# Performance work log

Measured on AMD Instinct MI355X. Metric: run time of the kernel, lower is better.

## Reference

```python
import jax, jax.numpy as jnp
import numpy as np

B, N, R, CIN = 2, 2048, 128, 256
RADIUS, NSAMPLE, OUT = 0.3, 16, 5
EPS = 1e-5


def setup_inputs():
    key = jax.random.key(0)
    ks = jax.random.split(key, 8)
    points_xyz = jax.random.uniform(ks[0], (B, N, 3)) * 2.0          # scene ~2m cube
    features = jax.random.normal(ks[1], (B, CIN, N))
    ctr = jax.random.uniform(ks[2], (B, R, 3)) * 2.0
    size = jax.random.uniform(ks[3], (B, R, 3)) * 0.6 + 0.3          # positive box sizes
    ang = jax.random.uniform(ks[4], (B, R, 1)) * np.pi
    rois = jnp.concatenate([ctr, size, ang], axis=-1)                # [B,R,7]
    s = 0.02
    W_mlp = jax.random.normal(ks[5], (256, CIN + 3)) * s
    g_mlp = jnp.ones((256,)); bt_mlp = jnp.zeros((256,))
    W1 = jax.random.normal(ks[6], (128, 256)) * s; b1 = jnp.zeros((128,))
    g1 = jnp.ones((128,)); bt1 = jnp.zeros((128,))
    W2 = jax.random.normal(ks[7], (128, 128)) * s; b2 = jnp.zeros((128,))
    g2 = jnp.ones((128,)); bt2 = jnp.zeros((128,))
    return dict(points_xyz=points_xyz, features=features, rois=rois,
                W_mlp=W_mlp, g_mlp=g_mlp, bt_mlp=bt_mlp,
                W1=W1, b1=b1, g1=g1, bt1=bt1,
                W2=W2, b2=b2, g2=g2, bt2=bt2)


def _bn(x, g, b, axes, shape):
    # training-mode BatchNorm (batch statistics), matching torch .train() forward
    m = jnp.mean(x, axes, keepdims=True)
    v = jnp.var(x, axes, keepdims=True)
    return (x - m) * jax.lax.rsqrt(v + EPS) * g.reshape(shape) + b.reshape(shape)


def _forward(points_xyz, features, rois, W_mlp, g_mlp, bt_mlp,
             W1, b1, g1, bt1, W2, b2, g2, bt2):
    # ---- QueryAndGroup: ball query (min_radius=0) + gather + center + normalize_xyz ----
    diff = points_xyz[:, :, None, :] - points_xyz[:, None, :, :]     # [B,Nq,Np,3]
    d2 = jnp.sum(diff * diff, -1)
    mask = d2 < RADIUS * RADIUS
    cand = jnp.where(mask, jnp.arange(N, dtype=jnp.int32)[None, None, :], N)
    idx = jnp.sort(cand, axis=-1)[..., :NSAMPLE]                     # first NSAMPLE in-ball, ascending point index
    idx = jnp.where(idx < N, idx, idx[..., :1])                      # pad with first valid (self always in-ball)
    gx = jax.vmap(lambda p, i: p[i])(points_xyz, idx)                # [B,N,S,3]
    gx = (gx - points_xyz[:, :, None, :]) / RADIUS                   # centered + normalized
    gf = jax.vmap(lambda f, i: f[i])(jnp.swapaxes(features, 1, 2), idx)  # [B,N,S,C]
    nf = jnp.transpose(jnp.concatenate([gx, gf], -1), (0, 3, 1, 2))  # [B,3+C,N,S] (use_xyz=True)
    # ---- mlp: Conv2d 1x1 (bias='auto' with BN -> no bias) + BN2d + ReLU ----
    h = jnp.einsum('oc,bcns->bons', W_mlp, nf)
    h = jax.nn.relu(_bn(h, g_mlp, bt_mlp, (0, 2, 3), (1, -1, 1, 1)))
    feats = jnp.max(h, -1)                                           # max_pool2d over samples -> [B,256,N]
    h = jnp.einsum('oc,bcn->bon', W1, feats) + b1[None, :, None]
    h = jax.nn.relu(_bn(h, g1, bt1, (0, 2), (1, -1, 1)))
    h = jnp.einsum('oc,bcn->bon', W2, h) + b2[None, :, None]
    feats = jax.nn.relu(_bn(h, g2, bt2, (0, 2), (1, -1, 1)))         # [B,128,N]
    # ---- RoIPool3d: roi-aware voxel max pool (out_size=5, mode='max') ----
    C = feats.shape[1]
    ctr, size, ry = rois[..., :3], rois[..., 3:6], rois[..., 6]
    rel = points_xyz[:, None, :, :] - ctr[:, :, None, :]             # [B,R,N,3]
    c = jnp.cos(ry)[:, :, None]; s = jnp.sin(ry)[:, :, None]
    lx = rel[..., 0] * c + rel[..., 1] * s                           # rotate by -ry into roi frame
    ly = -rel[..., 0] * s + rel[..., 1] * c
    local = jnp.stack([lx, ly, rel[..., 2]], -1)                     # [B,R,N,3]
    half = size[:, :, None, :] * 0.5
    inside = jnp.all(jnp.abs(local) < half, -1)                      # [B,R,N]
    v = jnp.clip(jnp.floor((local + half) / (2.0 * half) * OUT), 0, OUT - 1).astype(jnp.int32)
    vox = (v[..., 0] * OUT + v[..., 1]) * OUT + v[..., 2]
    base = jnp.arange(B * R, dtype=jnp.int32).reshape(B, R, 1) * (OUT ** 3)
    seg = jnp.where(inside, base + vox, B * R * OUT ** 3).reshape(-1)  # dummy segment for outside pts
    data = jnp.broadcast_to(jnp.swapaxes(feats, 1, 2)[:, None], (B, R, N, C)).reshape(-1, C)
    pooled = jax.ops.segment_max(data, seg, num_segments=B * R * OUT ** 3 + 1)[:-1]
    pooled = jnp.where(jnp.isneginf(pooled), 0.0, pooled)            # empty voxels -> 0
    roi_feats = pooled.reshape(B, R, OUT, OUT, OUT, C)
    return feats, roi_feats


def reference(points_xyz, features, rois, W_mlp, g_mlp, bt_mlp,
              W1, b1, g1, bt1, W2, b2, g2, bt2):
    return _forward(points_xyz, features, rois, W_mlp, g_mlp, bt_mlp,
                    W1, b1, g1, bt1, W2, b2, g2, bt2)
```

## Files before the change

kernel.cpp:

```cpp
#include <hip/hip_runtime.h>
#include <hip/hip_bf16.h>

typedef __hip_bfloat16 bf16;
typedef unsigned short u16;

#define NB   2
#define NPT  2048
#define NROI 128
#define CINF 256
#define NS   16
#define KDIM 259
#define KP2  288
#define C1   256
#define C2   128
#define NVOX 125
#define EPSF 1e-5f

typedef __bf16 bf16x8 __attribute__((ext_vector_type(8)));
typedef float  f32x4  __attribute__((ext_vector_type(4)));

__device__ __forceinline__ float ldin(const void* p, size_t i, int f32flag) {
    if (f32flag) return ((const float*)p)[i];
    unsigned short u = ((const unsigned short*)p)[i];
    return __uint_as_float(((unsigned)u) << 16);
}

__device__ __forceinline__ unsigned short f2bf(float x) {
    unsigned u = __float_as_uint(x);
    u += 0x7FFFu + ((u >> 16) & 1u);
    return (unsigned short)(u >> 16);
}

__device__ __forceinline__ int detect_flag(const void* __restrict__ Wm) {
    const uint4* p = (const uint4*)Wm;
    int bad = 0;
    #pragma unroll
    for (int i = 0; i < 8; i++) {
        uint4 v = p[i];
        unsigned w[4] = {v.x, v.y, v.z, v.w};
        #pragma unroll
        for (int j = 0; j < 4; j++) {
            if (!(fabsf(__uint_as_float(w[j] << 16)) <= 1e4f)) bad = 1;
            if (!(fabsf(__uint_as_float(w[j] & 0xFFFF0000u)) <= 1e4f)) bad = 1;
        }
    }
    return bad;
}


__global__ __launch_bounds__(256) void k_setup(
    const void* __restrict__ pts, const void* __restrict__ feat, const void* __restrict__ rois,
    const void* __restrict__ Wm, const void* __restrict__ gm, const void* __restrict__ btm,
    const void* __restrict__ W1, const void* __restrict__ b1, const void* __restrict__ g1,
    const void* __restrict__ bt1, const void* __restrict__ W2, const void* __restrict__ b2,
    const void* __restrict__ g2, const void* __restrict__ bt2,
    float* __restrict__ ptsf, float* __restrict__ roisf, float* __restrict__ params,
    u16* __restrict__ wbf, u16* __restrict__ w1bf, u16* __restrict__ w2bf,
    float* __restrict__ stats, u16* __restrict__ ftbf,
    float* __restrict__ psx, float* __restrict__ psy, float* __restrict__ psz) {
    int f = detect_flag(Wm);
    int bx = blockIdx.x;
    int tid = threadIdx.x;
    if (bx < 1024) {
        __shared__ float tile[32][33];
        int b = bx >> 9;
        int r = bx & 511;
        int n0 = (r & 63) * 32, c0 = (r >> 6) * 32;
        int tx = tid & 31, ty = tid >> 5;
        #pragma unroll
        for (int d = 0; d < 4; d++) {
            int c = c0 + ty + d * 8;
            tile[ty + d * 8][tx] = ldin(feat, ((size_t)(b * CINF + c)) * NPT + n0 + tx, f);
        }
        __syncthreads();
        #pragma unroll
        for (int d = 0; d < 4; d++) {
            int n = n0 + ty + d * 8;
            ftbf[((size_t)(b * NPT + n)) * CINF + c0 + tx] = f2bf(tile[tx][ty + d * 8]);
        }
    } else if (bx < 1312) {
        int e = (bx - 1024) * 256 + tid;
        int o = e / KP2, k = e % KP2;
        float v = 0.f;
        if (k < 256)      v = ldin(Wm, (size_t)o * KDIM + 3 + k, f);
        else if (k < 259) v = ldin(Wm, (size_t)o * KDIM + (k - 256), f);
        wbf[e] = f2bf(v);
    } else if (bx < 1440) {
        int e = (bx - 1312) * 256 + tid;
        w1bf[e] = f2bf(ldin(W1, e, f));
    } else if (bx < 1504) {
        int e = (bx - 1440) * 256 + tid;
        w2bf[e] = f2bf(ldin(W2, e, f));
    } else if (bx < 1552) {
        int e = (bx - 1504) * 256 + tid;
        if (e < NB * NPT * 3) ptsf[e] = ldin(pts, e, f);
    } else if (bx < 1559) {
        int e = (bx - 1552) * 256 + tid;
        if (e < NB * NROI * 7) roisf[e] = ldin(rois, e, f);
    } else if (bx < 1567) {
        int t = bx - 1559;
        const void* src; int off, n;
        switch (t) {
            case 0: src = gm;  off = 0;     n = 256; break;
            case 1: src = btm; off = 256;   n = 256; break;
            case 2: src = b1;  off = 33280; n = 128; break;
            case 3: src = g1;  off = 33408; n = 128; break;
            case 4: src = bt1; off = 33536; n = 128; break;
            case 5: src = b2;  off = 50048; n = 128; break;
            case 6: src = g2;  off = 50176; n = 128; break;
            default: src = bt2; off = 50304; n = 128; break;
        }
        if (tid < n) params[off + tid] = ldin(src, tid, f);
    } else if (bx < 1570) {
        int e = (bx - 1567) * 256 + tid;
        if (e < 768) {
            int d = e >> 8, o = e & 255;
            params[25088 + e] = ldin(Wm, (size_t)o * KDIM + d, f);
        }
    } else if (bx < 1586) {
        int e = (bx - 1570) * 256 + tid;
        if (e < NB * NPT) {
            psx[e] = ptsf ? ldin(pts, e * 3 + 0, f) : 0.f;
            psy[e] = ldin(pts, e * 3 + 1, f);
            psz[e] = ldin(pts, e * 3 + 2, f);
        }
    } else {
        int e = (bx - 1586) * 256 + tid;
        if (e < 1024) stats[e] = 0.f;
    }
}

__global__ __launch_bounds__(256) void k_qd(const float* __restrict__ psx, const float* __restrict__ psy,
                                            const float* __restrict__ psz, int* __restrict__ idxb,
                                            const u16* __restrict__ ftbf, const u16* __restrict__ wbf,
                                            float* __restrict__ Hf) {
    int bx = blockIdx.x;
    if (bx < 1024) {
        #pragma clang fp contract(off)
        int wid = threadIdx.x >> 6, lane = threadIdx.x & 63;
        int q = bx * 4 + wid;
        int b = q >> 11;
        int base = b * NPT;
        float qx = psx[q], qy = psy[q], qz = psz[q];
        const float R2 = (float)(0.3 * 0.3);
        size_t ob = (size_t)q * NS;
        int cnt = 0, j0 = -1;
        unsigned long long below = (lane == 63) ? ~0ull >> 1 : ((1ull << (lane + 1)) - 1) >> 1;
        for (int c0 = 0; c0 < NPT; c0 += 64) {
            int j = c0 + lane;
            float dx = qx - psx[base + j];
            float dy = qy - psy[base + j];
            float dz = qz - psz[base + j];
            float d2 = dx * dx + dy * dy + dz * dz;
            bool hit = d2 < R2;
            unsigned long long m = __ballot(hit);
            if (m) {
                if (j0 < 0) j0 = c0 + __builtin_ctzll(m);
                int pos = cnt + __popcll(m & below);
                if (hit && pos < NS) idxb[ob + pos] = j;
                cnt += __popcll(m);
            }
            if (cnt >= NS) break;
        }
        if (lane >= cnt && lane < NS) idxb[ob + lane] = j0;
    } else {
        int bx2 = bx - 1024;
        int w = threadIdx.x >> 6, lane = threadIdx.x & 63;
        int lg = lane >> 4, lr = lane & 15;
        int rbase = (bx2 & 255) * 16;
        int c0 = (bx2 >> 8) * 128 + w * 32;

        size_t aoff  = (size_t)(rbase + lr) * CINF + lg * 8;
        size_t boff0 = (size_t)(c0 + lr) * KP2 + lg * 8;
        size_t boff1 = (size_t)(c0 + 16 + lr) * KP2 + lg * 8;

        f32x4 acc0 = (f32x4){0.f, 0.f, 0.f, 0.f};
        f32x4 acc1 = (f32x4){0.f, 0.f, 0.f, 0.f};
        #pragma unroll
        for (int k0 = 0; k0 < 256; k0 += 32) {
            bf16x8 af = __builtin_bit_cast(bf16x8, *(const uint4*)(ftbf + aoff + k0));
            bf16x8 b0 = __builtin_bit_cast(bf16x8, *(const uint4*)(wbf + boff0 + k0));
            bf16x8 b1 = __builtin_bit_cast(bf16x8, *(const uint4*)(wbf + boff1 + k0));
            acc0 = __builtin_amdgcn_mfma_f32_16x16x32_bf16(af, b0, acc0, 0, 0, 0);
            acc1 = __builtin_amdgcn_mfma_f32_16x16x32_bf16(af, b1, acc1, 0, 0, 0);
        }
        #pragma unroll
        for (int r = 0; r < 4; r++) {
            int row = rbase + lg * 4 + r;
            Hf[(size_t)row * C1 + c0 + lr] = acc0[r];
            Hf[(size_t)row * C1 + c0 + 16 + lr] = acc1[r];
        }
    }
}

#define GPTS 8
__global__ __launch_bounds__(256) void k_gather(const float* __restrict__ Hf, const int* __restrict__ idxb,
                                                const float* __restrict__ ptsf, const float* __restrict__ wxyz,
                                                float* __restrict__ Hmax, float* __restrict__ Hmin,
                                                float* __restrict__ stats) {
    __shared__ int   lj[NS];
    __shared__ float lgx[NS], lgy[NS], lgz[NS];
    int o = threadIdx.x;
    float wx = wxyz[o], wy = wxyz[256 + o], wz = wxyz[512 + o];
    float ssum = 0.f, ssq = 0.f;
    for (int p = 0; p < GPTS; p++) {
        int pt = blockIdx.x * GPTS + p;
        int b = pt >> 11;
        int base = b * NPT;
        if (o < NS) {
            int j = idxb[(size_t)pt * NS + o];
            lj[o] = j;
            size_t jb = ((size_t)(base + j)) * 3;
            size_t cb = (size_t)pt * 3;
            lgx[o] = (ptsf[jb]     - ptsf[cb])     / 0.3f;
            lgy[o] = (ptsf[jb + 1] - ptsf[cb + 1]) / 0.3f;
            lgz[o] = (ptsf[jb + 2] - ptsf[cb + 2]) / 0.3f;
        }
        __syncthreads();
        float mx = -3.4e38f, mn = 3.4e38f;
        #pragma unroll
        for (int s = 0; s < NS; s++) {
            float v = Hf[(size_t)(base + lj[s]) * C1 + o] + wx * lgx[s] + wy * lgy[s] + wz * lgz[s];
            mx = fmaxf(mx, v); mn = fminf(mn, v);
            ssum += v; ssq += v * v;
        }
        Hmax[(size_t)pt * C1 + o] = mx;
        Hmin[(size_t)pt * C1 + o] = mn;
        __syncthreads();
    }
    atomicAdd(&stats[o], ssum);
    atomicAdd(&stats[256 + o], ssq);
}

__global__ __launch_bounds__(256) void k_lin1f(const float* __restrict__ Hmax, const float* __restrict__ Hmin,
                                               const float* __restrict__ stats, const float* __restrict__ g,
                                               const float* __restrict__ bt, const u16* __restrict__ Wb,
                                               const float* __restrict__ bias, float* __restrict__ out,
                                               float* __restrict__ sum, float* __restrict__ sumsq) {
    __shared__ __align__(16) u16 xa[16][264];
    int tid = threadIdx.x;
    int rbase = blockIdx.x * 16;
    {
        int c = tid;
        const float inv = 1.f / 65536.f;
        float m = stats[c] * inv;
        float var = fmaxf(stats[256 + c] * inv - m * m, 0.f);
        float a = g[c] / sqrtf(var + EPSF);
        float d = bt[c] - m * a;
        #pragma unroll
        for (int r = 0; r < 16; r++) {
            size_t e = (size_t)(rbase + r) * C1 + c;
            float h = (a > 0.f) ? Hmax[e] : Hmin[e];
            xa[r][c] = f2bf(fmaxf(a * h + d, 0.f));
        }
    }
    __syncthreads();
    int w = tid >> 6, lane = tid & 63;
    int lg = lane >> 4, lr = lane & 15;
    int c0 = w * 32;
    size_t boff0 = (size_t)(c0 + lr) * 256 + lg * 8;
    size_t boff1 = (size_t)(c0 + 16 + lr) * 256 + lg * 8;

    f32x4 acc0 = (f32x4){0.f, 0.f, 0.f, 0.f};
    f32x4 acc1 = (f32x4){0.f, 0.f, 0.f, 0.f};
    #pragma unroll
    for (int k0 = 0; k0 < 256; k0 += 32) {
        bf16x8 af = __builtin_bit_cast(bf16x8, *(const uint4*)&xa[lr][k0 + lg * 8]);
        bf16x8 b0 = __builtin_bit_cast(bf16x8, *(const uint4*)(Wb + boff0 + k0));
        bf16x8 b1 = __builtin_bit_cast(bf16x8, *(const uint4*)(Wb + boff1 + k0));
        acc0 = __builtin_amdgcn_mfma_f32_16x16x32_bf16(af, b0, acc0, 0, 0, 0);
        acc1 = __builtin_amdgcn_mfma_f32_16x16x32_bf16(af, b1, acc1, 0, 0, 0);
    }
    #pragma unroll
    for (int ct = 0; ct < 2; ct++) {
        f32x4 a = ct ? acc1 : acc0;
        int col = c0 + ct * 16 + lr;
        float bi = bias[col];
        float s = 0.f, q = 0.f;
        #pragma unroll
        for (int r = 0; r < 4; r++) {
            float h = a[r] + bi;
            out[(size_t)(rbase + lg * 4 + r) * C2 + col] = h;
            s += h; q += h * h;
        }
        s += __shfl_xor(s, 16); s += __shfl_xor(s, 32);
        q += __shfl_xor(q, 16); q += __shfl_xor(q, 32);
        if (lane < 16) {
            atomicAdd(&sum[col], s);
            atomicAdd(&sumsq[col], q);
        }
    }
}

__global__ __launch_bounds__(256) void k_lin2f(const float* __restrict__ h1, const float* __restrict__ stats1,
                                               const float* __restrict__ g, const float* __restrict__ bt,
                                               const u16* __restrict__ Wb, const float* __restrict__ bias,
                                               float* __restrict__ out, float* __restrict__ sum,
                                               float* __restrict__ sumsq) {
    __shared__ __align__(16) u16 xa[16][136];
    int tid = threadIdx.x;
    int rbase = blockIdx.x * 16;
    {
        int c = tid & 127, half = tid >> 7;
        const float inv = 1.f / 4096.f;
        float m = stats1[c] * inv;
        float var = fmaxf(stats1[128 + c] * inv - m * m, 0.f);
        float a = g[c] / sqrtf(var + EPSF);
        float d = bt[c] - m * a;
        #pragma unroll
        for (int rr = 0; rr < 8; rr++) {
            int r = half * 8 + rr;
            float h = h1[(size_t)(rbase + r) * C2 + c];
            xa[r][c] = f2bf(fmaxf(a * h + d, 0.f));
        }
    }
    __syncthreads();
    int w = tid >> 6, lane = tid & 63;
    int lg = lane >> 4, lr = lane & 15;
    int c0 = w * 32;
    size_t boff0 = (size_t)(c0 + lr) * 128 + lg * 8;
    size_t boff1 = (size_t)(c0 + 16 + lr) * 128 + lg * 8;

    f32x4 acc0 = (f32x4){0.f, 0.f, 0.f, 0.f};
    f32x4 acc1 = (f32x4){0.f, 0.f, 0.f, 0.f};
    #pragma unroll
    for (int k0 = 0; k0 < 128; k0 += 32) {
        bf16x8 af = __builtin_bit_cast(bf16x8, *(const uint4*)&xa[lr][k0 + lg * 8]);
        bf16x8 b0 = __builtin_bit_cast(bf16x8, *(const uint4*)(Wb + boff0 + k0));
        bf16x8 b1 = __builtin_bit_cast(bf16x8, *(const uint4*)(Wb + boff1 + k0));
        acc0 = __builtin_amdgcn_mfma_f32_16x16x32_bf16(af, b0, acc0, 0, 0, 0);
        acc1 = __builtin_amdgcn_mfma_f32_16x16x32_bf16(af, b1, acc1, 0, 0, 0);
    }
    #pragma unroll
    for (int ct = 0; ct < 2; ct++) {
        f32x4 a = ct ? acc1 : acc0;
        int col = c0 + ct * 16 + lr;
        float bi = bias[col];
        float s = 0.f, q = 0.f;
        #pragma unroll
        for (int r = 0; r < 4; r++) {
            float h = a[r] + bi;
            out[(size_t)(rbase + lg * 4 + r) * C2 + col] = h;
            s += h; q += h * h;
        }
        s += __shfl_xor(s, 16); s += __shfl_xor(s, 32);
        q += __shfl_xor(q, 16); q += __shfl_xor(q, 32);
        if (lane < 16) {
            atomicAdd(&sum[col], s);
            atomicAdd(&sumsq[col], q);
        }
    }
}

__global__ void k_final(const float* __restrict__ h2, const float* __restrict__ sum,
                        const float* __restrict__ sumsq, const float* __restrict__ g,
                        const float* __restrict__ bt, float* __restrict__ fp,
                        void* __restrict__ out0, const void* __restrict__ Wm) {
    int e = blockIdx.x * 256 + threadIdx.x;
    if (e >= NB * NPT * C2) return;
    int f = detect_flag(Wm);
    int o = e & (C2 - 1);
    int bn = e >> 7;
    int b = bn >> 11, n = bn & (NPT - 1);
    const float inv = 1.f / 4096.f;
    float m = sum[o] * inv;
    float var = fmaxf(sumsq[o] * inv - m * m, 0.f);
    float a = g[o] / sqrtf(var + EPSF);
    float d = bt[o] - m * a;
    float v = fmaxf(a * h2[e] + d, 0.f);
    fp[e] = v;
    size_t oi = ((size_t)(b * C2 + o)) * NPT + n;
    if (f) ((float*)out0)[oi] = v;
    else   ((unsigned short*)out0)[oi] = f2bf(v);
}

__global__ __launch_bounds__(512) void k_pool2(const float* __restrict__ ptsf, const float* __restrict__ roisf,
                                               const float* __restrict__ fp, void* __restrict__ d_out,
                                               const void* __restrict__ Wm, int* __restrict__ glist) {
    #pragma clang fp contract(off)
    __shared__ int pooled[NVOX * C2];
    __shared__ int cnt;
    __shared__ float rp[8];
    int f = detect_flag(Wm);
    int bid = blockIdx.x;
    int b = bid >> 7;
    int tid = threadIdx.x;
    for (int k = tid; k < NVOX * C2; k += 512) pooled[k] = 0;
    if (tid == 0) {
        cnt = 0;
        size_t rb = ((size_t)bid) * 7;
        rp[0] = roisf[rb];     rp[1] = roisf[rb + 1]; rp[2] = roisf[rb + 2];
        rp[3] = roisf[rb + 3] * 0.5f;
        rp[4] = roisf[rb + 4] * 0.5f;
        rp[5] = roisf[rb + 5] * 0.5f;
        float ry = roisf[rb + 6];
        rp[6] = (float)cos((double)ry);
        rp[7] = (float)sin((double)ry);
    }
    __syncthreads();
    float cx = rp[0], cy = rp[1], cz = rp[2];
    float hx = rp[3], hy = rp[4], hz = rp[5];
    float cf = rp[6], sf = rp[7];
    int* mylist = glist + bid * NPT;
    for (int n = tid; n < NPT; n += 512) {
        size_t pb = ((size_t)(b * NPT + n)) * 3;
        float rx  = ptsf[pb]     - cx;
        float ryy = ptsf[pb + 1] - cy;
        float rz  = ptsf[pb + 2] - cz;
        float lx = rx * cf + ryy * sf;
        float ly = -rx * sf + ryy * cf;
        if (fabsf(lx) < hx && fabsf(ly) < hy && fabsf(rz) < hz) {
            int vx = (int)fminf(fmaxf(floorf((lx + hx) / (2.f * hx) * 5.f), 0.f), 4.f);
            int vy = (int)fminf(fmaxf(floorf((ly + hy) / (2.f * hy) * 5.f), 0.f), 4.f);
            int vz = (int)fminf(fmaxf(floorf((rz + hz) / (2.f * hz) * 5.f), 0.f), 4.f);
            int vox = (vx * 5 + vy) * 5 + vz;
            int pos = atomicAdd(&cnt, 1);
            mylist[pos] = (vox << 16) | n;
        }
    }
    __syncthreads();
    int m = cnt;
    int c = tid & 127, slot = tid >> 7;
    for (int e = slot; e < m; e += 4) {
        int u = mylist[e];
        int n = u & 0xFFFF, vox = u >> 16;
        float v = fp[((size_t)(b * NPT + n)) * C2 + c];
        atomicMax(&pooled[vox * C2 + c], __float_as_int(v));
    }
    __syncthreads();
    size_t ob = (size_t)524288 + (size_t)bid * (NVOX * C2);
    for (int k = tid; k < NVOX * C2; k += 512) {
        float v = __int_as_float(pooled[k]);
        if (f) ((float*)d_out)[ob + k] = v;
        else   ((unsigned short*)d_out)[ob + k] = f2bf(v);
    }
}

extern "C" void kernel_launch(void* const* d_in, const int* in_sizes, int n_in,
                              void* d_out, int out_size, void* d_ws, size_t ws_size,
                              hipStream_t stream) {
    const void* pts  = d_in[0];
    const void* feat = d_in[1];
    const void* rois = d_in[2];
    const void* Wm   = d_in[3];
    const void* gm   = d_in[4];
    const void* btm  = d_in[5];
    const void* W1   = d_in[6];
    const void* b1   = d_in[7];
    const void* g1   = d_in[8];
    const void* bt1  = d_in[9];
    const void* W2   = d_in[10];
    const void* b2   = d_in[11];
    const void* g2   = d_in[12];
    const void* bt2  = d_in[13];

    float* ws     = (float*)d_ws;
    float* ptsf   = ws + 16;
    float* roisf  = ws + 12304;
    float* params = ws + 14096;
    u16*   w1bf   = (u16*)(params + 512);
    u16*   w2bf   = (u16*)(params + 512 + 16384);
    float* wxyz   = params + 25088;
    u16*   wbf    = (u16*)(ws + 64528);
    float* stats  = ws + 101392;
    int*   idxb   = (int*)(ws + 102416);
    u16*   ftbf   = (u16*)(ws + 167952);
    float* Hmax   = ws + 1216528;
    float* Hmin   = ws + 2265104;
    float* h1     = ws + 1216528;
    float* h2     = ws + 2265104;
    float* fp     = ws + 2789392;
    float* psx    = ws + 3313680;
    float* psy    = ws + 3317776;
    float* psz    = ws + 3321872;
    float* Hf     = ws + 3325968;
    int*   glist  = (int*)(ws + 3325968);

    k_setup<<<1590, 256, 0, stream>>>(pts, feat, rois, Wm, gm, btm, W1, b1, g1, bt1,
                                      W2, b2, g2, bt2, ptsf, roisf, params,
                                      wbf, w1bf, w2bf, stats, ftbf, psx, psy, psz);
    k_qd<<<1536, 256, 0, stream>>>(psx, psy, psz, idxb, ftbf, wbf, Hf);
    k_gather<<<(NB * NPT) / GPTS, 256, 0, stream>>>(Hf, idxb, ptsf, wxyz, Hmax, Hmin, stats);
    k_lin1f<<<256, 256, 0, stream>>>(Hmax, Hmin, stats, params + 0, params + 256,
                                     w1bf, params + 33280, h1, stats + 512, stats + 640);
    k_lin2f<<<256, 256, 0, stream>>>(h1, stats + 512, params + 33408, params + 33536,
                                     w2bf, params + 50048, h2, stats + 768, stats + 896);
    k_final<<<(NB * NPT * C2) / 256, 256, 0, stream>>>(h2, stats + 768, stats + 896,
                                                       params + 50176, params + 50304, fp, d_out, Wm);
    k_pool2<<<NB * NROI, 512, 0, stream>>>(ptsf, roisf, fp, d_out, Wm, glist);
}
```

Before: 181.9 us.

## Transpose final output via shared tile, vectorize pool writes, drop gather syncs

The final BN+ReLU kernel now stages a 64x64 tile in shared memory so that writes to the channel-major output are coalesced instead of strided. The gather kernel drops its shared-memory staging and barriers, and each thread loads the neighbor indices and coordinates itself. The pool kernel clears and writes out with 16-byte vectors. The ball-query loop is unrolled and loses its early exit, so it always scans all points, which adds work for queries that fill early. It also removes a pointer test on the x-coordinate load.

Measured after the change: 196.7 us. 8.1% more time.

```diff
diff --git a/kernel.cpp b/kernel.cpp
--- a/kernel.cpp
+++ b/kernel.cpp
@@ -120,7 +120,7 @@
     } else if (bx < 1586) {
         int e = (bx - 1570) * 256 + tid;
         if (e < NB * NPT) {
-            psx[e] = ptsf ? ldin(pts, e * 3 + 0, f) : 0.f;
+            psx[e] = ldin(pts, e * 3 + 0, f);
             psy[e] = ldin(pts, e * 3 + 1, f);
             psz[e] = ldin(pts, e * 3 + 2, f);
         }
@@ -146,6 +146,7 @@
         size_t ob = (size_t)q * NS;
         int cnt = 0, j0 = -1;
         unsigned long long below = (lane == 63) ? ~0ull >> 1 : ((1ull << (lane + 1)) - 1) >> 1;
+        #pragma unroll 4
         for (int c0 = 0; c0 < NPT; c0 += 64) {
             int j = c0 + lane;
             float dx = qx - psx[base + j];
@@ -160,7 +161,6 @@
                 if (hit && pos < NS) idxb[ob + pos] = j;
                 cnt += __popcll(m);
             }
-            if (cnt >= NS) break;
         }
         if (lane >= cnt && lane < NS) idxb[ob + lane] = j0;
     } else {
@@ -198,35 +198,34 @@
                                                 const float* __restrict__ ptsf, const float* __restrict__ wxyz,
                                                 float* __restrict__ Hmax, float* __restrict__ Hmin,
                                                 float* __restrict__ stats) {
-    __shared__ int   lj[NS];
-    __shared__ float lgx[NS], lgy[NS], lgz[NS];
     int o = threadIdx.x;
     float wx = wxyz[o], wy = wxyz[256 + o], wz = wxyz[512 + o];
     float ssum = 0.f, ssq = 0.f;
+    #pragma unroll
     for (int p = 0; p < GPTS; p++) {
         int pt = blockIdx.x * GPTS + p;
         int b = pt >> 11;
         int base = b * NPT;
-        if (o < NS) {
-            int j = idxb[(size_t)pt * NS + o];
-            lj[o] = j;
+        size_t cb = (size_t)pt * 3;
+        float cxx = ptsf[cb], cyy = ptsf[cb + 1], czz = ptsf[cb + 2];
+        float v[NS];
+        #pragma unroll
+        for (int s = 0; s < NS; s++) {
+            int j = idxb[(size_t)pt * NS + s];
             size_t jb = ((size_t)(base + j)) * 3;
-            size_t cb = (size_t)pt * 3;
-            lgx[o] = (ptsf[jb]     - ptsf[cb])     / 0.3f;
-            lgy[o] = (ptsf[jb + 1] - ptsf[cb + 1]) / 0.3f;
-            lgz[o] = (ptsf[jb + 2] - ptsf[cb + 2]) / 0.3f;
-        }
-        __syncthreads();
+            float gx = (ptsf[jb]     - cxx) / 0.3f;
+            float gy = (ptsf[jb + 1] - cyy) / 0.3f;
+            float gz = (ptsf[jb + 2] - czz) / 0.3f;
+            v[s] = Hf[(size_t)(base + j) * C1 + o] + wx * gx + wy * gy + wz * gz;
+        }
         float mx = -3.4e38f, mn = 3.4e38f;
         #pragma unroll
         for (int s = 0; s < NS; s++) {
-            float v = Hf[(size_t)(base + lj[s]) * C1 + o] + wx * lgx[s] + wy * lgy[s] + wz * lgz[s];
-            mx = fmaxf(mx, v); mn = fminf(mn, v);
-            ssum += v; ssq += v * v;
+            mx = fmaxf(mx, v[s]); mn = fminf(mn, v[s]);
+            ssum += v[s]; ssq += v[s] * v[s];
         }
         Hmax[(size_t)pt * C1 + o] = mx;
         Hmin[(size_t)pt * C1 + o] = mn;
-        __syncthreads();
     }
     atomicAdd(&stats[o], ssum);
     atomicAdd(&stats[256 + o], ssq);
@@ -352,40 +351,62 @@
     }
 }
 
-__global__ void k_final(const float* __restrict__ h2, const float* __restrict__ sum,
-                        const float* __restrict__ sumsq, const float* __restrict__ g,
-                        const float* __restrict__ bt, float* __restrict__ fp,
-                        void* __restrict__ out0, const void* __restrict__ Wm) {
-    int e = blockIdx.x * 256 + threadIdx.x;
-    if (e >= NB * NPT * C2) return;
+__global__ __launch_bounds__(256) void k_final2(const float* __restrict__ h2, const float* __restrict__ sum,
+                                                const float* __restrict__ sumsq, const float* __restrict__ g,
+                                                const float* __restrict__ bt, float* __restrict__ fp,
+                                                void* __restrict__ out0, const void* __restrict__ Wm) {
+    __shared__ float tile[64][65];
+    __shared__ float aL[64], dL[64];
     int f = detect_flag(Wm);
-    int o = e & (C2 - 1);
-    int bn = e >> 7;
-    int b = bn >> 11, n = bn & (NPT - 1);
-    const float inv = 1.f / 4096.f;
-    float m = sum[o] * inv;
-    float var = fmaxf(sumsq[o] * inv - m * m, 0.f);
-    float a = g[o] / sqrtf(var + EPSF);
-    float d = bt[o] - m * a;
-    float v = fmaxf(a * h2[e] + d, 0.f);
-    fp[e] = v;
-    size_t oi = ((size_t)(b * C2 + o)) * NPT + n;
-    if (f) ((float*)out0)[oi] = v;
-    else   ((unsigned short*)out0)[oi] = f2bf(v);
+    int bx = blockIdx.x;
+    int b = bx >> 6;
+    int rem = bx & 63;
+    int n0 = (rem >> 1) * 64;
+    int o0 = (rem & 1) * 64;
+    int tid = threadIdx.x;
+    if (tid < 64) {
+        int o = o0 + tid;
+        const float inv = 1.f / 4096.f;
+        float m = sum[o] * inv;
+        float var = fmaxf(sumsq[o] * inv - m * m, 0.f);
+        float a = g[o] / sqrtf(var + EPSF);
+        aL[tid] = a;
+        dL[tid] = bt[o] - m * a;
+    }
+    __syncthreads();
+    #pragma unroll
+    for (int it = 0; it < 16; it++) {
+        int idx = it * 256 + tid;
+        int nn = idx >> 6, oo = idx & 63;
+        size_t e = (size_t)(b * NPT + n0 + nn) * C2 + o0 + oo;
+        float v = fmaxf(aL[oo] * h2[e] + dL[oo], 0.f);
+        fp[e] = v;
+        tile[nn][oo] = v;
+    }
+    __syncthreads();
+    #pragma unroll
+    for (int it = 0; it < 16; it++) {
+        int idx = it * 256 + tid;
+        int oo = idx >> 6, nn = idx & 63;
+        size_t oi = ((size_t)(b * C2 + o0 + oo)) * NPT + n0 + nn;
+        float v = tile[nn][oo];
+        if (f) ((float*)out0)[oi] = v;
+        else   ((unsigned short*)out0)[oi] = f2bf(v);
+    }
 }
 
 __global__ __launch_bounds__(512) void k_pool2(const float* __restrict__ ptsf, const float* __restrict__ roisf,
                                                const float* __restrict__ fp, void* __restrict__ d_out,
                                                const void* __restrict__ Wm, int* __restrict__ glist) {
     #pragma clang fp contract(off)
-    __shared__ int pooled[NVOX * C2];
+    __shared__ __align__(16) int pooled[NVOX * C2];
     __shared__ int cnt;
     __shared__ float rp[8];
     int f = detect_flag(Wm);
     int bid = blockIdx.x;
     int b = bid >> 7;
     int tid = threadIdx.x;
-    for (int k = tid; k < NVOX * C2; k += 512) pooled[k] = 0;
+    for (int k = tid; k < NVOX * C2 / 4; k += 512) ((int4*)pooled)[k] = (int4){0, 0, 0, 0};
     if (tid == 0) {
         cnt = 0;
         size_t rb = ((size_t)bid) * 7;
@@ -429,10 +450,19 @@
     }
     __syncthreads();
     size_t ob = (size_t)524288 + (size_t)bid * (NVOX * C2);
-    for (int k = tid; k < NVOX * C2; k += 512) {
-        float v = __int_as_float(pooled[k]);
-        if (f) ((float*)d_out)[ob + k] = v;
-        else   ((unsigned short*)d_out)[ob + k] = f2bf(v);
+    if (f) {
+        for (int k4 = tid; k4 < NVOX * C2 / 4; k4 += 512) {
+            int4 w = ((const int4*)pooled)[k4];
+            float4 v = {__int_as_float(w.x), __int_as_float(w.y), __int_as_float(w.z), __int_as_float(w.w)};
+            *(float4*)((float*)d_out + ob + k4 * 4) = v;
+        }
+    } else {
+        for (int k4 = tid; k4 < NVOX * C2 / 4; k4 += 512) {
+            int4 w = ((const int4*)pooled)[k4];
+            ushort4 v = {f2bf(__int_as_float(w.x)), f2bf(__int_as_float(w.y)),
+                         f2bf(__int_as_float(w.z)), f2bf(__int_as_float(w.w))};
+            *(ushort4*)((unsigned short*)d_out + ob + k4 * 4) = v;
+        }
     }
 }
 
@@ -485,7 +515,7 @@
                                      w1bf, params + 33280, h1, stats + 512, stats + 640);
     k_lin2f<<<256, 256, 0, stream>>>(h1, stats + 512, params + 33408, params + 33536,
                                      w2bf, params + 50048, h2, stats + 768, stats + 896);
-    k_final<<<(NB * NPT * C2) / 256, 256, 0, stream>>>(h2, stats + 768, stats + 896,
-                                                       params + 50176, params + 50304, fp, d_out, Wm);
+    k_final2<<<128, 256, 0, stream>>>(h2, stats + 768, stats + 896,
+                                      params + 50176, params + 50304, fp, d_out, Wm);
     k_pool2<<<NB * NROI, 512, 0, stream>>>(ptsf, roisf, fp, d_out, Wm, glist);
 }
```
